# Optimization experiments

Hardware: AMD Instinct MI355X
Metric: run time of the kernel (lower is better)

## Reference

```python
import jax, jax.numpy as jnp
import numpy as np

N_ENTITIES = 200000
N_USERS = 100000
DIM = 64
N_EDGES = 1000000
N_INTER = 1000000
N_REL = 33
N_INTERACTION_TYPES = 8


def segment_softmax(x, seg, num_segments):
    # two-pass numerically stable segment softmax (torch_scatter.scatter_softmax)
    m = jax.ops.segment_max(x, seg, num_segments=num_segments)
    e = jnp.exp(x - m[seg])
    s = jax.ops.segment_sum(e, seg, num_segments=num_segments)
    return e / s[seg]


def setup_inputs() -> dict:
    key = jax.random.key(0)
    ks = jax.random.split(key, 9)
    return {
        "entity_emb": jax.random.normal(ks[0], (N_ENTITIES, DIM), dtype=jnp.float32),
        "user_emb": jax.random.normal(ks[1], (N_USERS, DIM), dtype=jnp.float32),
        "interaction_emb": jax.random.normal(ks[2], (N_INTERACTION_TYPES, DIM), dtype=jnp.float32),
        "relation_emb": jax.random.normal(ks[3], (N_REL, DIM), dtype=jnp.float32),
        "edge_index": jax.random.randint(ks[4], (2, N_EDGES), 0, N_ENTITIES, dtype=jnp.int32),
        "edge_type": jax.random.randint(ks[5], (N_EDGES,), 1, N_REL, dtype=jnp.int32),
        "user_index": jax.random.randint(ks[6], (N_INTER,), 0, N_USERS, dtype=jnp.int32),
        "item_index": jax.random.randint(ks[7], (N_INTER,), 0, N_ENTITIES, dtype=jnp.int32),
        "interact_type": jax.random.randint(ks[8], (N_INTER,), 0, N_INTERACTION_TYPES, dtype=jnp.int32),
    }


def reference(entity_emb, user_emb, interaction_emb, relation_emb,
              edge_index, edge_type, user_index, item_index, interact_type):
    n_entities = entity_emb.shape[0]
    n_users = user_emb.shape[0]
    head, tail = edge_index[0], edge_index[1]

    # --- entity aggregation over KG edges ---
    neigh = entity_emb[tail]                                      # [E, D]
    w1 = jnp.sum(neigh * relation_emb[edge_type - 1], axis=1) / 8.0   # [E]
    w1 = segment_softmax(w1, head, n_entities)[:, None]           # [E, 1]
    entity_agg = jax.ops.segment_sum(neigh * w1, head, num_segments=n_entities)  # [n_entities, D]

    # --- user aggregation over interactions (agg_method='attention') ---
    interact_entity_emb = entity_emb[item_index]                  # [I, D]
    att = jnp.sum(interaction_emb[interact_type] * user_emb[user_index] * interact_entity_emb, axis=1)  # [I]
    att_w = segment_softmax(att, user_index, n_users)[:, None]    # [I, 1]
    user_agg = jax.ops.segment_sum(att_w * interact_entity_emb, user_index, num_segments=n_users)  # [n_users, D]

    return entity_agg, user_agg, att_w, w1
```

## Files before the change

kernel.cpp:

```cpp
#include <hip/hip_runtime.h>
#include <hip/hip_bf16.h>

#define DIM 64
#define RELS 32
#define SCAN_B 512
#define TILE_V 64

__global__ __launch_bounds__(256, 4) void buildM_deg(
    const float* __restrict__ ent, const float* __restrict__ rel,
    __hip_bfloat16* __restrict__ M,
    const int* __restrict__ head, const int* __restrict__ uidx,
    unsigned int* __restrict__ degP,
    unsigned char* __restrict__ rank_e, unsigned char* __restrict__ rank_i,
    int nE, int E, int I, int gM) {
    __shared__ float4 entL[TILE_V * 17];
    __shared__ float relS[4][16][33];
    int tx = threadIdx.x;
    int bid = blockIdx.x;

    if (bid >= gM) {
        int t = (bid - gM) * 256 + tx;
        if (t < E) {
            int s = head[t];
            unsigned int old = atomicAdd(&degP[s >> 2], 1u << (8 * (s & 3)));
            rank_e[t] = (unsigned char)((old >> (8 * (s & 3))) & 0xFFu);
        } else if (t < E + I) {
            int e = t - E;
            int s = nE + uidx[e];
            unsigned int old = atomicAdd(&degP[s >> 2], 1u << (8 * (s & 3)));
            rank_i[e] = (unsigned char)((old >> (8 * (s & 3))) & 0xFFu);
        }
        return;
    }

    int vg = tx >> 4, rg = tx & 15;
    int base = bid * TILE_V;
    const float4* rel4 = (const float4*)rel;
    #pragma unroll
    for (int k = 0; k < 2; k++) {
        int idx = tx + k * 256;
        float4 v = rel4[idx];
        int r = idx >> 4, d4 = idx & 15;
        relS[0][d4][r] = v.x; relS[1][d4][r] = v.y;
        relS[2][d4][r] = v.z; relS[3][d4][r] = v.w;
    }
    const float4* ent4 = (const float4*)ent;
    #pragma unroll
    for (int k = 0; k < 4; k++) {
        int idx = tx + k * 256;
        int row = idx >> 4, col = idx & 15;
        int v = base + row;
        entL[row * 17 + col] = (v < nE) ? ent4[(size_t)v * 16 + col]
                                        : make_float4(0.f, 0.f, 0.f, 0.f);
    }
    __syncthreads();

    float acc[4][2] = {{0.f,0.f},{0.f,0.f},{0.f,0.f},{0.f,0.f}};
    int r0 = rg * 2;
    #pragma unroll 2
    for (int d4 = 0; d4 < 16; d4++) {
        float4 a0 = entL[(vg * 4 + 0) * 17 + d4];
        float4 a1 = entL[(vg * 4 + 1) * 17 + d4];
        float4 a2 = entL[(vg * 4 + 2) * 17 + d4];
        float4 a3 = entL[(vg * 4 + 3) * 17 + d4];
        float bx0 = relS[0][d4][r0],     by0 = relS[1][d4][r0];
        float bz0 = relS[2][d4][r0],     bw0 = relS[3][d4][r0];
        float bx1 = relS[0][d4][r0 + 1], by1 = relS[1][d4][r0 + 1];
        float bz1 = relS[2][d4][r0 + 1], bw1 = relS[3][d4][r0 + 1];
        acc[0][0] = fmaf(a0.x,bx0, fmaf(a0.y,by0, fmaf(a0.z,bz0, fmaf(a0.w,bw0, acc[0][0]))));
        acc[1][0] = fmaf(a1.x,bx0, fmaf(a1.y,by0, fmaf(a1.z,bz0, fmaf(a1.w,bw0, acc[1][0]))));
        acc[2][0] = fmaf(a2.x,bx0, fmaf(a2.y,by0, fmaf(a2.z,bz0, fmaf(a2.w,bw0, acc[2][0]))));
        acc[3][0] = fmaf(a3.x,bx0, fmaf(a3.y,by0, fmaf(a3.z,bz0, fmaf(a3.w,bw0, acc[3][0]))));
        acc[0][1] = fmaf(a0.x,bx1, fmaf(a0.y,by1, fmaf(a0.z,bz1, fmaf(a0.w,bw1, acc[0][1]))));
        acc[1][1] = fmaf(a1.x,bx1, fmaf(a1.y,by1, fmaf(a1.z,bz1, fmaf(a1.w,bw1, acc[1][1]))));
        acc[2][1] = fmaf(a2.x,bx1, fmaf(a2.y,by1, fmaf(a2.z,bz1, fmaf(a2.w,bw1, acc[2][1]))));
        acc[3][1] = fmaf(a3.x,bx1, fmaf(a3.y,by1, fmaf(a3.z,bz1, fmaf(a3.w,bw1, acc[3][1]))));
    }
    __hip_bfloat162* M2 = (__hip_bfloat162*)M;
    #pragma unroll
    for (int i = 0; i < 4; i++) {
        int v = base + vg * 4 + i;
        if (v < nE) {
            __hip_bfloat16 h0 = __float2bfloat16(acc[i][0] * 0.125f);
            __hip_bfloat16 h1 = __float2bfloat16(acc[i][1] * 0.125f);
            M2[(size_t)v * 16 + rg] = __halves2bfloat162(h0, h1);
        }
    }
}

__global__ __launch_bounds__(SCAN_B) void scan_partial(
    const unsigned int* __restrict__ degP, unsigned int* __restrict__ part, int nW) {
    __shared__ unsigned int lds[SCAN_B];
    int i = blockIdx.x * SCAN_B + threadIdx.x;
    unsigned int v = (i < nW) ? degP[i] : 0u;
    lds[threadIdx.x] = (v & 0xFFu) + ((v >> 8) & 0xFFu) + ((v >> 16) & 0xFFu) + (v >> 24);
    __syncthreads();
    for (int off = SCAN_B >> 1; off > 0; off >>= 1) {
        if (threadIdx.x < off) lds[threadIdx.x] += lds[threadIdx.x + off];
        __syncthreads();
    }
    if (threadIdx.x == 0) part[blockIdx.x] = lds[0];
}

__global__ __launch_bounds__(1024) void scan_block(unsigned int* __restrict__ part, int nb) {
    __shared__ unsigned int lds[1024];
    int t = threadIdx.x;
    unsigned int v = (t < nb) ? part[t] : 0u;
    lds[t] = v;
    __syncthreads();
    for (int off = 1; off < 1024; off <<= 1) {
        unsigned int x = (t >= off) ? lds[t - off] : 0u;
        __syncthreads();
        lds[t] += x;
        __syncthreads();
    }
    if (t < nb) part[t] = lds[t] - v;
}

__global__ __launch_bounds__(SCAN_B) void scan_final(
    const unsigned int* __restrict__ degP, const unsigned int* __restrict__ part,
    unsigned int* __restrict__ offs, int nW) {
    __shared__ unsigned int lds[SCAN_B];
    int t = threadIdx.x;
    int i = blockIdx.x * SCAN_B + t;
    unsigned int v = (i < nW) ? degP[i] : 0u;
    unsigned int b0 = v & 0xFFu, b1 = (v >> 8) & 0xFFu, b2 = (v >> 16) & 0xFFu, b3 = v >> 24;
    unsigned int tot = b0 + b1 + b2 + b3;
    lds[t] = tot;
    __syncthreads();
    for (int off = 1; off < SCAN_B; off <<= 1) {
        unsigned int x = (t >= off) ? lds[t - off] : 0u;
        __syncthreads();
        lds[t] += x;
        __syncthreads();
    }
    if (i < nW) {
        unsigned int base = part[blockIdx.x] + lds[t] - tot;
        uint4 o;
        o.x = base; o.y = base + b0; o.z = base + b0 + b1; o.w = base + b0 + b1 + b2;
        ((uint4*)offs)[i] = o;
    }
}

__global__ __launch_bounds__(256) void scatter32(
    const int* __restrict__ head, const int* __restrict__ tail, const int* __restrict__ etype,
    const int* __restrict__ uidx, const int* __restrict__ iidx, const int* __restrict__ ttype,
    const unsigned char* __restrict__ rank_e, const unsigned char* __restrict__ rank_i,
    const unsigned int* __restrict__ offs,
    unsigned int* __restrict__ pay, unsigned int* __restrict__ payu,
    int E, int I, int nE) {
    int t = blockIdx.x * blockDim.x + threadIdx.x;
    if (t < E) {
        unsigned int p = offs[head[t]] + rank_e[t];
        unsigned int v = (unsigned int)tail[t] | ((unsigned int)(etype[t] - 1) << 18);
        __builtin_nontemporal_store(v, &pay[p]);
    } else if (t < E + I) {
        int e = t - E;
        unsigned int p = offs[nE + uidx[e]] + rank_i[e] - (unsigned)E;
        unsigned int v = (unsigned int)iidx[e] | ((unsigned int)ttype[e] << 27);
        __builtin_nontemporal_store(v, &payu[p]);
    }
}

__global__ __launch_bounds__(256) void fused_agg(
    const float* __restrict__ ent, const float* __restrict__ usr,
    const float* __restrict__ itc, const __hip_bfloat16* __restrict__ M,
    const unsigned int* __restrict__ pay, const unsigned int* __restrict__ payu,
    const unsigned int* __restrict__ degP, const unsigned int* __restrict__ offs,
    float* __restrict__ patt, float2* __restrict__ msum,
    float* __restrict__ aggE, float* __restrict__ aggU,
    int nE, int nU, int E, int gAE) {
    __shared__ float4 itcL[8][16];
    int tx = threadIdx.x;
    int bid = blockIdx.x;

    if (bid < gAE) {
        int t = bid * 256 + tx;
        int h = t >> 4, l = t & 15;
        if (h >= nE) return;
        unsigned int d = (degP[h >> 2] >> (8 * (h & 3))) & 0xFFu;
        float m = -3.0e38f, s = 0.f, inv = 0.f;
        float4 acc = make_float4(0.f, 0.f, 0.f, 0.f);
        if (d) {
            unsigned int off = offs[h];
            unsigned int v0 = pay[off];
            float sc0 = __bfloat162float(M[(size_t)(v0 & 0x3FFFFu) * RELS + (v0 >> 18)]);
            float4 a0 = ((const float4*)(ent + (size_t)(v0 & 0x3FFFFu) * DIM))[l];
            for (unsigned int j = 0; j < d; j++) {
                float sc1 = sc0; float4 a1 = a0;
                if (j + 1 < d) {
                    unsigned int v1 = pay[off + j + 1];
                    sc1 = __bfloat162float(M[(size_t)(v1 & 0x3FFFFu) * RELS + (v1 >> 18)]);
                    a1 = ((const float4*)(ent + (size_t)(v1 & 0x3FFFFu) * DIM))[l];
                }
                float mn = fmaxf(m, sc0);
                float scale = __expf(m - mn);
                float w = __expf(sc0 - mn);
                s = s * scale + w;
                acc.x = acc.x * scale + w * a0.x;
                acc.y = acc.y * scale + w * a0.y;
                acc.z = acc.z * scale + w * a0.z;
                acc.w = acc.w * scale + w * a0.w;
                m = mn; sc0 = sc1; a0 = a1;
            }
            inv = 1.f / s;
        }
        if (l == 0) msum[h] = make_float2(m, inv);
        acc.x *= inv; acc.y *= inv; acc.z *= inv; acc.w *= inv;
        ((float4*)(aggE + (size_t)h * DIM))[l] = acc;
        return;
    }

    if (tx < 128) itcL[tx >> 4][tx & 15] = ((const float4*)itc)[tx];
    __syncthreads();
    int t = (bid - gAE) * 256 + tx;
    int h = t >> 4, l = t & 15;
    if (h >= nU) return;
    int hs = nE + h;
    unsigned int d = (degP[hs >> 2] >> (8 * (hs & 3))) & 0xFFu;
    float m = -3.0e38f, s = 0.f, inv = 0.f;
    float4 acc = make_float4(0.f, 0.f, 0.f, 0.f);
    float4 ur = ((const float4*)(usr + (size_t)h * DIM))[l];
    if (d) {
        unsigned int off = offs[hs] - (unsigned)E;
        unsigned int v0 = payu[off];
        float4 a0 = ((const float4*)(ent + (size_t)(v0 & 0x7ffffffu) * DIM))[l];
        for (unsigned int j = 0; j < d; j++) {
            unsigned int v1 = v0; float4 a1 = a0;
            if (j + 1 < d) {
                v1 = payu[off + j + 1];
                a1 = ((const float4*)(ent + (size_t)(v1 & 0x7ffffffu) * DIM))[l];
            }
            float4 c = itcL[v0 >> 27][l];
            float p = a0.x * ur.x * c.x + a0.y * ur.y * c.y
                    + a0.z * ur.z * c.z + a0.w * ur.w * c.w;
            p += __shfl_xor(p, 1);
            p += __shfl_xor(p, 2);
            p += __shfl_xor(p, 4);
            p += __shfl_xor(p, 8);
            if (l == 0) patt[off + j] = p;
            float mn = fmaxf(m, p);
            float scale = __expf(m - mn);
            float w = __expf(p - mn);
            s = s * scale + w;
            acc.x = acc.x * scale + w * a0.x;
            acc.y = acc.y * scale + w * a0.y;
            acc.z = acc.z * scale + w * a0.z;
            acc.w = acc.w * scale + w * a0.w;
            m = mn; v0 = v1; a0 = a1;
        }
        inv = 1.f / s;
    }
    if (l == 0) msum[hs] = make_float2(m, inv);
    acc.x *= inv; acc.y *= inv; acc.z *= inv; acc.w *= inv;
    ((float4*)(aggU + (size_t)h * DIM))[l] = acc;
}

__global__ __launch_bounds__(256) void wout(
    const int* __restrict__ head, const int* __restrict__ tail, const int* __restrict__ etype,
    const int* __restrict__ uidx,
    const __hip_bfloat16* __restrict__ M, const float* __restrict__ patt,
    const unsigned char* __restrict__ rank_i,
    const unsigned int* __restrict__ offs, const float2* __restrict__ msum,
    float* __restrict__ w1, float* __restrict__ attw, int E, int I, int nE) {
    int t = blockIdx.x * blockDim.x + threadIdx.x;
    if (t < E) {
        float2 mi = msum[head[t]];
        float sc = __bfloat162float(M[(size_t)tail[t] * RELS + (etype[t] - 1)]);
        w1[t] = __expf(sc - mi.x) * mi.y;
    } else if (t < E + I) {
        int e = t - E; int u = uidx[e];
        float2 mi = msum[nE + u];
        float sc = patt[offs[nE + u] - (unsigned)E + rank_i[e]];
        attw[e] = __expf(sc - mi.x) * mi.y;
    }
}

extern "C" void kernel_launch(void* const* d_in, const int* in_sizes, int n_in,
                              void* d_out, int out_size, void* d_ws, size_t ws_size,
                              hipStream_t stream) {
    const float* ent  = (const float*)d_in[0];
    const float* usr  = (const float*)d_in[1];
    const float* itc  = (const float*)d_in[2];
    const float* rel  = (const float*)d_in[3];
    const int* eidx   = (const int*)d_in[4];
    const int* etype  = (const int*)d_in[5];
    const int* uidx   = (const int*)d_in[6];
    const int* iidx   = (const int*)d_in[7];
    const int* ttype  = (const int*)d_in[8];

    const int E  = in_sizes[4] / 2;
    const int I  = in_sizes[6];
    const int nE = in_sizes[0] / DIM;
    const int nU = in_sizes[1] / DIM;
    const int* head = eidx;
    const int* tail = eidx + E;
    const int NSEG = nE + nU;
    const int NW = (NSEG + 3) / 4;
    const int NWpad = (NW + 3) & ~3;
    const int NB = (NW + SCAN_B - 1) / SCAN_B;

    float* out_entity = (float*)d_out;
    float* out_user   = out_entity + (size_t)nE * DIM;
    float* out_attw   = out_user + (size_t)nU * DIM;
    float* out_w1     = out_attw + I;

    unsigned int* degP    = (unsigned int*)d_ws;
    unsigned int* offs    = degP + NWpad;
    unsigned int* part    = offs + NSEG;
    unsigned char* rank_e = (unsigned char*)(part + 1024);
    unsigned char* rank_i = rank_e + E;
    unsigned int* pay     = (unsigned int*)(rank_i + I);
    unsigned int* payu    = pay + E;
    __hip_bfloat16* M     = (__hip_bfloat16*)(payu + I);
    float2* msum          = (float2*)(M + (size_t)nE * RELS);
    float* patt           = (float*)(msum + NSEG);

    hipMemsetAsync(degP, 0, (size_t)NWpad * sizeof(unsigned int), stream);

    const int T = 256;
    const int gM  = (nE + TILE_V - 1) / TILE_V;
    const int gD  = (E + I + T - 1) / T;
    const int gAE = (int)(((size_t)nE * 16 + T - 1) / T);
    const int gAU = (int)(((size_t)nU * 16 + T - 1) / T);

    buildM_deg<<<dim3((unsigned)(gM + gD)), T, 0, stream>>>(
        ent, rel, M, head, uidx, degP, rank_e, rank_i, nE, E, I, gM);

    scan_partial<<<dim3((unsigned)NB), SCAN_B, 0, stream>>>(degP, part, NW);
    scan_block<<<dim3(1), 1024, 0, stream>>>(part, NB);
    scan_final<<<dim3((unsigned)NB), SCAN_B, 0, stream>>>(degP, part, offs, NW);

    scatter32<<<dim3((unsigned)gD), T, 0, stream>>>(
        head, tail, etype, uidx, iidx, ttype, rank_e, rank_i, offs, pay, payu, E, I, nE);

    fused_agg<<<dim3((unsigned)(gAE + gAU)), T, 0, stream>>>(
        ent, usr, itc, M, pay, payu, degP, offs, patt, msum,
        out_entity, out_user, nE, nU, E, gAE);

    wout<<<dim3((unsigned)gD), T, 0, stream>>>(
        head, tail, etype, uidx, M, patt, rank_i, offs, msum, out_w1, out_attw, E, I, nE);
}
```

Measured before the change: 332.9 us.

## Precompute edge scores in scatter and gather bf16 entity rows in aggregation

buildM_deg now also writes a bf16 copy of the entity table. scatter32 looks up each edge's relation score once and stores it twice: in a 64-bit payload next to the tail index, and in a per-edge score array that wout reads directly. The entity aggregation loop reads the score straight from the payload and gathers half-width bf16 neighbor rows, so each dependent random access moves fewer bytes. The cost is extra writes (the bf16 table, wider payloads, the score array) and lower precision in the aggregated entity output.

```diff
diff --git a/kernel.cpp b/kernel.cpp
--- a/kernel.cpp
+++ b/kernel.cpp
@@ -6,9 +6,25 @@
 #define SCAN_B 512
 #define TILE_V 64
 
+__device__ __forceinline__ unsigned int pk_bf2(float a, float b) {
+    unsigned int ua = __float_as_uint(a);
+    unsigned int ub = __float_as_uint(b);
+    ua = (ua + 0x7fffu + ((ua >> 16) & 1u)) >> 16;
+    ub = (ub + 0x7fffu + ((ub >> 16) & 1u)) >> 16;
+    return ua | (ub << 16);
+}
+__device__ __forceinline__ float4 bf4_to_f4(uint2 u) {
+    float4 r;
+    r.x = __uint_as_float(u.x << 16);
+    r.y = __uint_as_float(u.x & 0xffff0000u);
+    r.z = __uint_as_float(u.y << 16);
+    r.w = __uint_as_float(u.y & 0xffff0000u);
+    return r;
+}
+
 __global__ __launch_bounds__(256, 4) void buildM_deg(
     const float* __restrict__ ent, const float* __restrict__ rel,
-    __hip_bfloat16* __restrict__ M,
+    __hip_bfloat16* __restrict__ M, uint2* __restrict__ entB2,
     const int* __restrict__ head, const int* __restrict__ uidx,
     unsigned int* __restrict__ degP,
     unsigned char* __restrict__ rank_e, unsigned char* __restrict__ rank_i,
@@ -50,8 +66,12 @@
         int idx = tx + k * 256;
         int row = idx >> 4, col = idx & 15;
         int v = base + row;
-        entL[row * 17 + col] = (v < nE) ? ent4[(size_t)v * 16 + col]
-                                        : make_float4(0.f, 0.f, 0.f, 0.f);
+        float4 val = make_float4(0.f, 0.f, 0.f, 0.f);
+        if (v < nE) {
+            val = ent4[(size_t)v * 16 + col];
+            entB2[(size_t)v * 16 + col] = make_uint2(pk_bf2(val.x, val.y), pk_bf2(val.z, val.w));
+        }
+        entL[row * 17 + col] = val;
     }
     __syncthreads();
 
@@ -143,17 +163,21 @@
 }
 
 __global__ __launch_bounds__(256) void scatter32(
+    const __hip_bfloat16* __restrict__ M,
     const int* __restrict__ head, const int* __restrict__ tail, const int* __restrict__ etype,
     const int* __restrict__ uidx, const int* __restrict__ iidx, const int* __restrict__ ttype,
     const unsigned char* __restrict__ rank_e, const unsigned char* __restrict__ rank_i,
     const unsigned int* __restrict__ offs,
-    unsigned int* __restrict__ pay, unsigned int* __restrict__ payu,
-    int E, int I, int nE) {
+    unsigned long long* __restrict__ pay64, unsigned int* __restrict__ payu,
+    float* __restrict__ e_sc, int E, int I, int nE) {
     int t = blockIdx.x * blockDim.x + threadIdx.x;
     if (t < E) {
+        int tl = tail[t];
+        float sc = __bfloat162float(M[(size_t)tl * RELS + (etype[t] - 1)]);
+        e_sc[t] = sc;
         unsigned int p = offs[head[t]] + rank_e[t];
-        unsigned int v = (unsigned int)tail[t] | ((unsigned int)(etype[t] - 1) << 18);
-        __builtin_nontemporal_store(v, &pay[p]);
+        unsigned long long v = ((unsigned long long)__float_as_uint(sc) << 32) | (unsigned int)tl;
+        __builtin_nontemporal_store(v, &pay64[p]);
     } else if (t < E + I) {
         int e = t - E;
         unsigned int p = offs[nE + uidx[e]] + rank_i[e] - (unsigned)E;
@@ -163,9 +187,9 @@
 }
 
 __global__ __launch_bounds__(256) void fused_agg(
-    const float* __restrict__ ent, const float* __restrict__ usr,
-    const float* __restrict__ itc, const __hip_bfloat16* __restrict__ M,
-    const unsigned int* __restrict__ pay, const unsigned int* __restrict__ payu,
+    const uint2* __restrict__ entB2, const float* __restrict__ ent,
+    const float* __restrict__ usr, const float* __restrict__ itc,
+    const unsigned long long* __restrict__ pay64, const unsigned int* __restrict__ payu,
     const unsigned int* __restrict__ degP, const unsigned int* __restrict__ offs,
     float* __restrict__ patt, float2* __restrict__ msum,
     float* __restrict__ aggE, float* __restrict__ aggU,
@@ -183,25 +207,25 @@
         float4 acc = make_float4(0.f, 0.f, 0.f, 0.f);
         if (d) {
             unsigned int off = offs[h];
-            unsigned int v0 = pay[off];
-            float sc0 = __bfloat162float(M[(size_t)(v0 & 0x3FFFFu) * RELS + (v0 >> 18)]);
-            float4 a0 = ((const float4*)(ent + (size_t)(v0 & 0x3FFFFu) * DIM))[l];
+            unsigned long long v0 = pay64[off];
+            uint2 b0 = entB2[(size_t)(unsigned int)(v0 & 0xffffffffu) * 16 + l];
             for (unsigned int j = 0; j < d; j++) {
-                float sc1 = sc0; float4 a1 = a0;
+                unsigned long long v1 = v0; uint2 b1 = b0;
                 if (j + 1 < d) {
-                    unsigned int v1 = pay[off + j + 1];
-                    sc1 = __bfloat162float(M[(size_t)(v1 & 0x3FFFFu) * RELS + (v1 >> 18)]);
-                    a1 = ((const float4*)(ent + (size_t)(v1 & 0x3FFFFu) * DIM))[l];
+                    v1 = pay64[off + j + 1];
+                    b1 = entB2[(size_t)(unsigned int)(v1 & 0xffffffffu) * 16 + l];
                 }
-                float mn = fmaxf(m, sc0);
+                float sc = __uint_as_float((unsigned int)(v0 >> 32));
+                float4 a0 = bf4_to_f4(b0);
+                float mn = fmaxf(m, sc);
                 float scale = __expf(m - mn);
-                float w = __expf(sc0 - mn);
+                float w = __expf(sc - mn);
                 s = s * scale + w;
                 acc.x = acc.x * scale + w * a0.x;
                 acc.y = acc.y * scale + w * a0.y;
                 acc.z = acc.z * scale + w * a0.z;
                 acc.w = acc.w * scale + w * a0.w;
-                m = mn; sc0 = sc1; a0 = a1;
+                m = mn; v0 = v1; b0 = b1;
             }
             inv = 1.f / s;
         }
@@ -257,17 +281,15 @@
 }
 
 __global__ __launch_bounds__(256) void wout(
-    const int* __restrict__ head, const int* __restrict__ tail, const int* __restrict__ etype,
-    const int* __restrict__ uidx,
-    const __hip_bfloat16* __restrict__ M, const float* __restrict__ patt,
+    const int* __restrict__ head, const int* __restrict__ uidx,
+    const float* __restrict__ e_sc, const float* __restrict__ patt,
     const unsigned char* __restrict__ rank_i,
     const unsigned int* __restrict__ offs, const float2* __restrict__ msum,
     float* __restrict__ w1, float* __restrict__ attw, int E, int I, int nE) {
     int t = blockIdx.x * blockDim.x + threadIdx.x;
     if (t < E) {
         float2 mi = msum[head[t]];
-        float sc = __bfloat162float(M[(size_t)tail[t] * RELS + (etype[t] - 1)]);
-        w1[t] = __expf(sc - mi.x) * mi.y;
+        w1[t] = __expf(e_sc[t] - mi.x) * mi.y;
     } else if (t < E + I) {
         int e = t - E; int u = uidx[e];
         float2 mi = msum[nE + u];
@@ -305,16 +327,18 @@
     float* out_attw   = out_user + (size_t)nU * DIM;
     float* out_w1     = out_attw + I;
 
-    unsigned int* degP    = (unsigned int*)d_ws;
-    unsigned int* offs    = degP + NWpad;
-    unsigned int* part    = offs + NSEG;
-    unsigned char* rank_e = (unsigned char*)(part + 1024);
-    unsigned char* rank_i = rank_e + E;
-    unsigned int* pay     = (unsigned int*)(rank_i + I);
-    unsigned int* payu    = pay + E;
-    __hip_bfloat16* M     = (__hip_bfloat16*)(payu + I);
-    float2* msum          = (float2*)(M + (size_t)nE * RELS);
-    float* patt           = (float*)(msum + NSEG);
+    unsigned int* degP      = (unsigned int*)d_ws;
+    unsigned int* offs      = degP + NWpad;
+    unsigned int* part      = offs + NSEG;
+    unsigned long long* pay64 = (unsigned long long*)(part + 1024);
+    unsigned int* payu      = (unsigned int*)(pay64 + E);
+    float* e_sc             = (float*)(payu + I);
+    __hip_bfloat16* M       = (__hip_bfloat16*)(e_sc + E);
+    uint2* entB2            = (uint2*)(M + (size_t)nE * RELS);
+    float2* msum            = (float2*)(entB2 + (size_t)nE * 16);
+    float* patt             = (float*)(msum + NSEG);
+    unsigned char* rank_e   = (unsigned char*)(patt + I);
+    unsigned char* rank_i   = rank_e + E;
 
     hipMemsetAsync(degP, 0, (size_t)NWpad * sizeof(unsigned int), stream);
 
@@ -325,19 +349,20 @@
     const int gAU = (int)(((size_t)nU * 16 + T - 1) / T);
 
     buildM_deg<<<dim3((unsigned)(gM + gD)), T, 0, stream>>>(
-        ent, rel, M, head, uidx, degP, rank_e, rank_i, nE, E, I, gM);
+        ent, rel, M, entB2, head, uidx, degP, rank_e, rank_i, nE, E, I, gM);
 
     scan_partial<<<dim3((unsigned)NB), SCAN_B, 0, stream>>>(degP, part, NW);
     scan_block<<<dim3(1), 1024, 0, stream>>>(part, NB);
     scan_final<<<dim3((unsigned)NB), SCAN_B, 0, stream>>>(degP, part, offs, NW);
 
     scatter32<<<dim3((unsigned)gD), T, 0, stream>>>(
-        head, tail, etype, uidx, iidx, ttype, rank_e, rank_i, offs, pay, payu, E, I, nE);
+        M, head, tail, etype, uidx, iidx, ttype, rank_e, rank_i, offs,
+        pay64, payu, e_sc, E, I, nE);
 
     fused_agg<<<dim3((unsigned)(gAE + gAU)), T, 0, stream>>>(
-        ent, usr, itc, M, pay, payu, degP, offs, patt, msum,
+        entB2, ent, usr, itc, pay64, payu, degP, offs, patt, msum,
         out_entity, out_user, nE, nU, E, gAE);
 
     wout<<<dim3((unsigned)gD), T, 0, stream>>>(
-        head, tail, etype, uidx, M, patt, rank_i, offs, msum, out_w1, out_attw, E, I, nE);
-}
+        head, uidx, e_sc, patt, rank_i, offs, msum, out_w1, out_attw, E, I, nE);
+}
```

Result: faster. 312.9 us (-6.0%).
